# Kernel optimization log

Hardware: AMD Instinct MI355X
Metric: run time of the kernel (lower is better)

The kernel has to match this reference:

```python
import jax, jax.numpy as jnp
import numpy as np

B, S, H, V = 2, 2048, 1024, 32000
SDS = [64, 128, 256]
EPS = 1e-5


def _ln(x, g, b):
    m = jnp.mean(x, -1, keepdims=True)
    v = jnp.var(x, -1, keepdims=True)
    return (x - m) * jax.lax.rsqrt(v + EPS) * g + b


def _layer(x, A_log, Wb, Wc, D, Wg, bg, Wo, bo, g, be):
    # x: [B,S,H]; state dim N = A_log.shape[0]
    A = jnp.exp(A_log)
    gate = jax.nn.sigmoid(jnp.einsum('bsh,nh->bsn', x, Wg) + bg)
    Bx = jnp.einsum('bsh,nh->bsn', x, Wb)
    u = gate * Bx  # [B,S,N]

    def step(s, u_t):
        s = A * s + u_t
        return s, s

    s0 = jnp.zeros((x.shape[0], A.shape[0]), x.dtype)
    _, states = jax.lax.scan(step, s0, jnp.swapaxes(u, 0, 1))  # [S,B,N]
    states = jnp.swapaxes(states, 0, 1)
    y = jnp.einsum('bsn,hn->bsh', states, Wc) + D * x
    out = _ln(y + x, g, be)
    return out @ Wo.T + bo  # dropout is identity (p used in eval / p=0)


def setup_inputs() -> dict:
    key = jax.random.key(0)
    ks = iter(jax.random.split(key, 64))
    d = {}
    d['x'] = jax.random.randint(next(ks), (B, S), 0, V)
    d['E'] = jax.random.normal(next(ks), (V, H), jnp.float32) * 0.02
    for i, N in enumerate(SDS):
        d[f'A{i}'] = jnp.log(jnp.exp(jnp.full((N,), -0.5)) + 0.1 * jax.random.normal(next(ks), (N,)))
        d[f'Wb{i}'] = jax.random.normal(next(ks), (N, H), jnp.float32) * 0.02
        d[f'Wc{i}'] = jax.random.normal(next(ks), (H, N), jnp.float32) * 0.02
        d[f'D{i}'] = jax.random.normal(next(ks), (H,), jnp.float32)
        d[f'Wg{i}'] = jax.random.normal(next(ks), (N, H), jnp.float32) * 0.02
        d[f'bg{i}'] = jnp.zeros((N,), jnp.float32)
        d[f'Wo{i}'] = jax.random.normal(next(ks), (H, H), jnp.float32) * 0.02
        d[f'bo{i}'] = jnp.zeros((H,), jnp.float32)
        d[f'g{i}'] = jnp.ones((H,), jnp.float32)
        d[f'be{i}'] = jnp.zeros((H,), jnp.float32)
    d['Wf'] = jax.random.normal(next(ks), (H, 3 * H), jnp.float32) * 0.02
    d['bf'] = jnp.zeros((H,), jnp.float32)
    d['gf'] = jnp.ones((H,), jnp.float32)
    d['bef'] = jnp.zeros((H,), jnp.float32)
    d['Wh'] = jax.random.normal(next(ks), (V, H), jnp.float32) * 0.02
    d['bh'] = jnp.zeros((V,), jnp.float32)
    return d


def reference(x, E,
              A0, Wb0, Wc0, D0, Wg0, bg0, Wo0, bo0, g0, be0,
              A1, Wb1, Wc1, D1, Wg1, bg1, Wo1, bo1, g1, be1,
              A2, Wb2, Wc2, D2, Wg2, bg2, Wo2, bo2, g2, be2,
              Wf, bf, gf, bef, Wh, bh):
    emb = E[x]  # [B,S,H]
    o0 = _layer(emb, A0, Wb0, Wc0, D0, Wg0, bg0, Wo0, bo0, g0, be0)
    o1 = _layer(emb, A1, Wb1, Wc1, D1, Wg1, bg1, Wo1, bo1, g1, be1)
    o2 = _layer(emb, A2, Wb2, Wc2, D2, Wg2, bg2, Wo2, bo2, g2, be2)
    combined = jnp.concatenate([o0, o1, o2], axis=-1)  # [B,S,3H]
    fused = combined @ Wf.T + bf
    fused = _ln(fused + emb, gf, bef)
    logits = fused @ Wh.T + bh  # [B,S,V]
    return logits
```

## Files before the change

### kernel.cpp

```cpp
#include <hip/hip_runtime.h>
#include <hip/hip_bf16.h>

#define Hd 1024
#define Bdim 2
#define Sd 2048
#define BSd 4096
#define Vd 32000
#define EPSf 1e-5f
#define CH 16
#define NCH 128
#define NT3 448

typedef __attribute__((ext_vector_type(8))) short short8;
typedef __attribute__((ext_vector_type(4))) float f32x4;
typedef __attribute__((ext_vector_type(4))) unsigned short us4;

__device__ __forceinline__ unsigned short f2bf(float f) {
  union { float f; unsigned int u; } v; v.f = f;
  return (unsigned short)((v.u + 0x7fffu + ((v.u >> 16) & 1u)) >> 16);
}

typedef __attribute__((address_space(1))) const void gvoid_t;
typedef __attribute__((address_space(3))) void svoid_t;
__device__ __forceinline__ void gl_lds16(const void* g, void* s) {
  __builtin_amdgcn_global_load_lds((gvoid_t*)g, (svoid_t*)s, 16, 0, 0);
}

struct CvtTab {
  const float* src[14];
  unsigned short* dst[14];
  int start[15];
};
__global__ void k_cvt_all(CvtTab tab) {
  int b = blockIdx.x;
  int j = 0;
  while (j < 13 && b >= tab.start[j + 1]) ++j;
  size_t i = (size_t)(b - tab.start[j]) * 256 + threadIdx.x;
  f32x4 v = *(const f32x4*)(tab.src[j] + i * 4);
  us4 o;
  o[0] = f2bf(v[0]); o[1] = f2bf(v[1]); o[2] = f2bf(v[2]); o[3] = f2bf(v[3]);
  *(us4*)(tab.dst[j] + i * 4) = o;
}

__global__ void k_setup(const float* A0, const float* A1, const float* A2,
                        const float* b0, const float* b1, const float* b2,
                        const float* D0, const float* D1, const float* D2,
                        const float* g0, const float* g1, const float* g2,
                        const float* e0, const float* e1, const float* e2,
                        float* Alog448, float* bg448,
                        float* D3, float* g3, float* be3) {
  int t = blockIdx.x * 256 + threadIdx.x;
  if (t < NT3) {
    int l = t < 64 ? 0 : (t < 192 ? 1 : 2);
    int o = t - (l == 0 ? 0 : (l == 1 ? 64 : 192));
    Alog448[t] = (l == 0 ? A0 : (l == 1 ? A1 : A2))[o];
    bg448[t]   = (l == 0 ? b0 : (l == 1 ? b1 : b2))[o];
  }
  if (t < 3072) {
    int l = t >> 10, o = t & 1023;
    D3[t]  = (l == 0 ? D0 : (l == 1 ? D1 : D2))[o];
    g3[t]  = (l == 0 ? g0 : (l == 1 ? g1 : g2))[o];
    be3[t] = (l == 0 ? e0 : (l == 1 ? e1 : e2))[o];
  }
}

__global__ void k_embed(const int* __restrict__ x, const float* __restrict__ E,
                        float* __restrict__ emb, unsigned short* __restrict__ embbf) {
  int row = blockIdx.x, t = threadIdx.x;
  int id = x[row];
  f32x4 v = *(const f32x4*)(E + (size_t)id * Hd + t * 4);
  *(f32x4*)(emb + (size_t)row * Hd + t * 4) = v;
  us4 o;
  o[0] = f2bf(v[0]); o[1] = f2bf(v[1]); o[2] = f2bf(v[2]); o[3] = f2bf(v[3]);
  *(us4*)(embbf + (size_t)row * Hd + t * 4) = o;
}

template<int BM, int BN, int WM, int WN, int BF16_OUT>
__launch_bounds__(WM * WN * 64)
__global__ void gemm2ph(const unsigned short* __restrict__ A,
                        const unsigned short* __restrict__ Bw,
                        const float* __restrict__ bias,
                        void* __restrict__ Cv,
                        int N, int K, int lda, int ldb, int ldc, int coff, int tm)
{
  constexpr int NT = WM * WN * 64;
  constexpr int MF = BM / WM / 16;
  constexpr int NF = BN / WN / 16;
  constexpr int ASZ = BM * 64;
  constexpr int BSZ = BN * 64;
  constexpr int AR = (ASZ * 2) / (NT * 16);
  constexpr int BR = (BSZ * 2) / (NT * 16);
  __shared__ __align__(16) unsigned short Sm[2 * (ASZ + BSZ)];

  int T = gridDim.x;
  int orig = blockIdx.x;
  int q = T >> 3, r = T & 7;
  int xc = orig & 7, sdv = orig >> 3;
  int wgid = (xc < r ? xc * (q + 1) : r * (q + 1) + (xc - r) * q) + sdv;
  int n_t = wgid / tm, m_t = wgid % tm;
  int row0 = m_t * BM, col0 = n_t * BN;

  int tid = threadIdx.x;
  int wave = tid >> 6, lane = tid & 63;
  int wm = wave / WN, wn = wave % WN;
  int wr = wm * (BM / WM), wc = wn * (BN / WN);
  int lr = lane & 15;
  int klane = lane >> 4;

  f32x4 acc[MF][NF] = {};

  auto stage = [&](int buf, int k0) {
    unsigned short* Ab = Sm + buf * (ASZ + BSZ);
    unsigned short* Bb = Ab + ASZ;
    #pragma unroll
    for (int j = 0; j < AR; ++j) {
      int slot = j * NT + tid;
      int lrow = slot >> 3, c16 = slot & 7;
      int scol = (c16 ^ (lrow & 7)) * 8;
      gl_lds16(A + (size_t)(row0 + lrow) * lda + k0 + scol, Ab + (j * NT + wave * 64) * 8);
    }
    #pragma unroll
    for (int j = 0; j < BR; ++j) {
      int slot = j * NT + tid;
      int lrow = slot >> 3, c16 = slot & 7;
      int scol = (c16 ^ (lrow & 7)) * 8;
      int brow = col0 + lrow;
      if (brow >= N) brow = N - 1;
      gl_lds16(Bw + (size_t)brow * ldb + k0 + scol, Bb + (j * NT + wave * 64) * 8);
    }
  };

  auto compute = [&](int buf) {
    const unsigned short* Ab = Sm + buf * (ASZ + BSZ);
    const unsigned short* Bb = Ab + ASZ;
    #pragma unroll
    for (int kk = 0; kk < 2; ++kk) {
      short8 afr[MF], bfr[NF];
      #pragma unroll
      for (int m = 0; m < MF; ++m) {
        int row = wr + m * 16 + lr;
        int cs = (kk * 4 + klane) ^ (row & 7);
        afr[m] = *(const short8*)(Ab + row * 64 + cs * 8);
      }
      #pragma unroll
      for (int n = 0; n < NF; ++n) {
        int row = wc + n * 16 + lr;
        int cs = (kk * 4 + klane) ^ (row & 7);
        bfr[n] = *(const short8*)(Bb + row * 64 + cs * 8);
      }
      #pragma unroll
      for (int m = 0; m < MF; ++m)
        #pragma unroll
        for (int n = 0; n < NF; ++n)
          acc[m][n] = __builtin_amdgcn_mfma_f32_16x16x32_bf16(afr[m], bfr[n], acc[m][n], 0, 0, 0);
    }
  };

  int nt = K >> 6;
  stage(0, 0);
  __syncthreads();
  for (int t = 0; t < nt - 1; ++t) {
    stage((t & 1) ^ 1, (t + 1) * 64);
    compute(t & 1);
    __syncthreads();
  }
  compute((nt - 1) & 1);

  int rb = (lane >> 4) * 4;
  #pragma unroll
  for (int m = 0; m < MF; ++m) {
    #pragma unroll
    for (int n = 0; n < NF; ++n) {
      int gcol = col0 + wc + n * 16 + lr;
      if (gcol >= N) continue;
      float bv = bias ? bias[gcol] : 0.f;
      #pragma unroll
      for (int j = 0; j < 4; ++j) {
        int grow = row0 + wr + m * 16 + rb + j;
        float val = acc[m][n][j] + bv;
        if (BF16_OUT)
          ((unsigned short*)Cv)[(size_t)grow * ldc + coff + gcol] = f2bf(val);
        else
          ((float*)Cv)[(size_t)grow * ldc + coff + gcol] = val;
      }
    }
  }
}

__global__ void k_scanA(const float* __restrict__ gzbx, const float* __restrict__ Alog448,
                        const float* __restrict__ bg448,
                        float* __restrict__ st, float* __restrict__ carry) {
  int gid = blockIdx.x * 256 + threadIdx.x;
  if (gid >= Bdim * NCH * NT3) return;
  int n = gid % NT3;
  int c = (gid / NT3) % NCH;
  int b = gid / (NT3 * NCH);
  float a = expf(Alog448[n]);
  float bgv = bg448[n];
  float s = 0.f;
  size_t rbase = (size_t)b * Sd + (size_t)c * CH;
  for (int t = 0; t < CH; ++t) {
    size_t row = rbase + t;
    float gzv = gzbx[row * 896 + n];
    float bxv = gzbx[row * 896 + 448 + n];
    float gv = 1.f / (1.f + expf(-(gzv + bgv)));
    s = a * s + gv * bxv;
    st[row * NT3 + n] = s;
  }
  carry[((size_t)b * NCH + c) * NT3 + n] = s;
}

__global__ void k_scanB(const float* __restrict__ carry, const float* __restrict__ Alog448,
                        float* __restrict__ cin) {
  int i = blockIdx.x * 256 + threadIdx.x;
  if (i >= Bdim * NT3) return;
  int b = i / NT3, n = i % NT3;
  float aC = expf((float)CH * Alog448[n]);
  float s = 0.f;
  for (int c = 0; c < NCH; ++c) {
    cin[((size_t)b * NCH + c) * NT3 + n] = s;
    s = aC * s + carry[((size_t)b * NCH + c) * NT3 + n];
  }
}

__global__ void k_scanC(const float* __restrict__ st, const float* __restrict__ cin,
                        const float* __restrict__ Alog448, unsigned short* __restrict__ stbf) {
  size_t gid = (size_t)blockIdx.x * 256 + threadIdx.x;
  if (gid >= (size_t)BSd * NT3) return;
  int n = gid % NT3;
  int row = gid / NT3;
  int b = row / Sd, sg = row % Sd;
  int c = sg / CH, t = sg % CH;
  float cv = cin[((size_t)b * NCH + c) * NT3 + n];
  float val = st[gid] + expf((float)(t + 1) * Alog448[n]) * cv;
  stbf[gid] = f2bf(val);
}

__global__ void k_ln3(const float* __restrict__ y3, const float* __restrict__ emb,
                      const float* __restrict__ D3, const float* __restrict__ g3,
                      const float* __restrict__ be3, unsigned short* __restrict__ z3) {
  int row = blockIdx.x, ly = blockIdx.y, t = threadIdx.x;
  const float* y = y3 + (size_t)row * 3072 + ly * 1024;
  f32x4 yv = *(const f32x4*)(y + t * 4);
  f32x4 ev = *(const f32x4*)(emb + (size_t)row * Hd + t * 4);
  float vals[4];
  float sum = 0.f, sq = 0.f;
  #pragma unroll
  for (int j = 0; j < 4; ++j) {
    float coef = D3[ly * 1024 + t * 4 + j] + 1.f;
    float v = yv[j] + coef * ev[j];
    vals[j] = v; sum += v; sq += v * v;
  }
  #pragma unroll
  for (int o = 32; o >= 1; o >>= 1) {
    sum += __shfl_xor(sum, o);
    sq += __shfl_xor(sq, o);
  }
  __shared__ float red[2][4];
  int w = t >> 6, lane = t & 63;
  if (lane == 0) { red[0][w] = sum; red[1][w] = sq; }
  __syncthreads();
  sum = red[0][0] + red[0][1] + red[0][2] + red[0][3];
  sq  = red[1][0] + red[1][1] + red[1][2] + red[1][3];
  float mean = sum * (1.f / Hd);
  float var = sq * (1.f / Hd) - mean * mean;
  float rs = rsqrtf(var + EPSf);
  us4 o4;
  #pragma unroll
  for (int j = 0; j < 4; ++j) {
    float z = (vals[j] - mean) * rs * g3[ly * 1024 + t * 4 + j] + be3[ly * 1024 + t * 4 + j];
    o4[j] = f2bf(z);
  }
  *(us4*)(z3 + (size_t)row * 3072 + ly * 1024 + t * 4) = o4;
}

__global__ void k_ln(const float* __restrict__ y, const float* __restrict__ emb,
                     const float* __restrict__ g, const float* __restrict__ be,
                     unsigned short* __restrict__ out) {
  int row = blockIdx.x, t = threadIdx.x;
  f32x4 yv = *(const f32x4*)(y + (size_t)row * Hd + t * 4);
  f32x4 ev = *(const f32x4*)(emb + (size_t)row * Hd + t * 4);
  float vals[4];
  float sum = 0.f, sq = 0.f;
  #pragma unroll
  for (int j = 0; j < 4; ++j) {
    float v = yv[j] + ev[j];
    vals[j] = v; sum += v; sq += v * v;
  }
  #pragma unroll
  for (int o = 32; o >= 1; o >>= 1) {
    sum += __shfl_xor(sum, o);
    sq += __shfl_xor(sq, o);
  }
  __shared__ float red[2][4];
  int w = t >> 6, lane = t & 63;
  if (lane == 0) { red[0][w] = sum; red[1][w] = sq; }
  __syncthreads();
  sum = red[0][0] + red[0][1] + red[0][2] + red[0][3];
  sq  = red[1][0] + red[1][1] + red[1][2] + red[1][3];
  float mean = sum * (1.f / Hd);
  float var = sq * (1.f / Hd) - mean * mean;
  float rs = rsqrtf(var + EPSf);
  us4 o4;
  #pragma unroll
  for (int j = 0; j < 4; ++j) {
    float z = (vals[j] - mean) * rs * g[t * 4 + j] + be[t * 4 + j];
    o4[j] = f2bf(z);
  }
  *(us4*)(out + (size_t)row * Hd + t * 4) = o4;
}

extern "C" void kernel_launch(void* const* d_in, const int* in_sizes, int n_in,
                              void* d_out, int out_size, void* d_ws, size_t ws_size,
                              hipStream_t stream) {
  (void)in_sizes; (void)n_in; (void)out_size; (void)ws_size;
  const int* x = (const int*)d_in[0];
  const float* E = (const float*)d_in[1];
  const float* Wf_ = (const float*)d_in[32];
  const float* bfb = (const float*)d_in[33];
  const float* gfp = (const float*)d_in[34];
  const float* bef = (const float*)d_in[35];
  const float* Wh_ = (const float*)d_in[36];
  const float* bh = (const float*)d_in[37];

  char* wsb = (char*)d_ws;
  size_t off = 0;
  auto alloc = [&](size_t bytes) -> void* {
    void* p = wsb + off;
    off += (bytes + 255) & ~(size_t)255;
    return p;
  };
  float* emb             = (float*)alloc((size_t)BSd * Hd * 4);
  unsigned short* embbf  = (unsigned short*)alloc((size_t)BSd * Hd * 2);
  unsigned short* wgwbbf = (unsigned short*)alloc((size_t)896 * Hd * 2);
  unsigned short* wcbf   = (unsigned short*)alloc((size_t)NT3 * Hd * 2);
  unsigned short* wobf   = (unsigned short*)alloc((size_t)3 * Hd * Hd * 2);
  unsigned short* wfbf   = (unsigned short*)alloc((size_t)3 * Hd * Hd * 2);
  unsigned short* whbf   = (unsigned short*)alloc((size_t)Vd * Hd * 2);
  float* gzbx            = (float*)alloc((size_t)BSd * 896 * 4);
  float* stl             = (float*)alloc((size_t)BSd * NT3 * 4);
  unsigned short* stbf   = (unsigned short*)alloc((size_t)BSd * NT3 * 2);
  float* carry           = (float*)alloc((size_t)Bdim * NCH * NT3 * 4);
  float* cin             = (float*)alloc((size_t)Bdim * NCH * NT3 * 4);
  float* ybuf3           = (float*)alloc((size_t)BSd * 3072 * 4);
  unsigned short* zbf3   = (unsigned short*)alloc((size_t)BSd * 3072 * 2);
  unsigned short* zbf    = (unsigned short*)alloc((size_t)BSd * Hd * 2);
  unsigned short* combbf = (unsigned short*)alloc((size_t)BSd * 3072 * 2);
  float* Alog448         = (float*)alloc(NT3 * 4);
  float* bg448           = (float*)alloc(NT3 * 4);
  float* D3              = (float*)alloc(3072 * 4);
  float* g3              = (float*)alloc(3072 * 4);
  float* be3             = (float*)alloc(3072 * 4);

  k_embed<<<BSd, 256, 0, stream>>>(x, E, emb, embbf);

  {
    CvtTab tab;
    const int rowoff_g[3] = {0, 64, 192};
    int j = 0;
    int n4s[14];
    for (int i = 0; i < 3; ++i) { tab.src[j] = (const float*)d_in[2 + 10 * i + 4]; tab.dst[j] = wgwbbf + (size_t)rowoff_g[i] * Hd;        n4s[j] = (64 << i) * Hd / 4; ++j; }
    for (int i = 0; i < 3; ++i) { tab.src[j] = (const float*)d_in[2 + 10 * i + 1]; tab.dst[j] = wgwbbf + (size_t)(448 + rowoff_g[i]) * Hd; n4s[j] = (64 << i) * Hd / 4; ++j; }
    for (int i = 0; i < 3; ++i) { tab.src[j] = (const float*)d_in[2 + 10 * i + 2]; tab.dst[j] = wcbf + (size_t)rowoff_g[i] * Hd;           n4s[j] = (64 << i) * Hd / 4; ++j; }
    for (int i = 0; i < 3; ++i) { tab.src[j] = (const float*)d_in[2 + 10 * i + 6]; tab.dst[j] = wobf + (size_t)i * Hd * Hd;                n4s[j] = Hd * Hd / 4; ++j; }
    tab.src[j] = Wf_; tab.dst[j] = wfbf; n4s[j] = 3 * Hd * Hd / 4; ++j;
    tab.src[j] = Wh_; tab.dst[j] = whbf; n4s[j] = Vd * Hd / 4; ++j;
    tab.start[0] = 0;
    for (int k = 0; k < 14; ++k) tab.start[k + 1] = tab.start[k] + (n4s[k] + 255) / 256;
    k_cvt_all<<<tab.start[14], 256, 0, stream>>>(tab);
  }

  k_setup<<<12, 256, 0, stream>>>(
      (const float*)d_in[2], (const float*)d_in[12], (const float*)d_in[22],
      (const float*)d_in[7], (const float*)d_in[17], (const float*)d_in[27],
      (const float*)d_in[5], (const float*)d_in[15], (const float*)d_in[25],
      (const float*)d_in[10], (const float*)d_in[20], (const float*)d_in[30],
      (const float*)d_in[11], (const float*)d_in[21], (const float*)d_in[31],
      Alog448, bg448, D3, g3, be3);

  const int TM = BSd / 128;

  gemm2ph<128,128,2,2,0><<<(896 / 128) * TM, 256, 0, stream>>>(
      embbf, wgwbbf, nullptr, gzbx, 896, Hd, Hd, Hd, 896, 0, TM);

  {
    int totA = Bdim * NCH * NT3;
    k_scanA<<<(totA + 255) / 256, 256, 0, stream>>>(gzbx, Alog448, bg448, stl, carry);
    k_scanB<<<(Bdim * NT3 + 255) / 256, 256, 0, stream>>>(carry, Alog448, cin);
    size_t totC = (size_t)BSd * NT3;
    k_scanC<<<(int)((totC + 255) / 256), 256, 0, stream>>>(stl, cin, Alog448, stbf);
  }

  const int owg[3] = {0, 64, 192};
  const int sd[3] = {64, 128, 256};
  for (int i = 0; i < 3; ++i) {
    gemm2ph<128,128,2,2,0><<<(Hd / 128) * TM, 256, 0, stream>>>(
        stbf + owg[i], wcbf + (size_t)owg[i] * Hd, nullptr, ybuf3,
        Hd, sd[i], NT3, sd[i], 3072, i * Hd, TM);
  }

  k_ln3<<<dim3(BSd, 3), 256, 0, stream>>>(ybuf3, emb, D3, g3, be3, zbf3);

  for (int i = 0; i < 3; ++i) {
    const float* bo = (const float*)d_in[2 + 10 * i + 7];
    gemm2ph<128,128,2,2,1><<<(Hd / 128) * TM, 256, 0, stream>>>(
        zbf3 + i * Hd, wobf + (size_t)i * Hd * Hd, bo, combbf,
        Hd, Hd, 3072, Hd, 3072, i * Hd, TM);
  }

  gemm2ph<128,128,2,2,0><<<(Hd / 128) * TM, 256, 0, stream>>>(
      combbf, wfbf, bfb, ybuf3, Hd, 3 * Hd, 3 * Hd, 3 * Hd, Hd, 0, TM);
  k_ln<<<BSd, 256, 0, stream>>>(ybuf3, emb, gfp, bef, zbf);

  const int TM256 = BSd / 256;
  gemm2ph<256,256,2,4,0><<<(Vd / 256) * TM256, 512, 0, stream>>>(
      zbf, whbf, bh, (float*)d_out, Vd, Hd, Hd, Hd, Vd, 0, TM256);
}
```

Measured before the change: 671.6 us.

## Fold per-layer output projections into fusion weights; add 4-stage pipelined vocab GEMM

Precomputes a combined weight Wf·blockdiag(Wo_i) and a combined bias (bf + Wf·bo), so the three per-layer 1024x1024 output GEMMs over 4096 tokens go away. Their cost is replaced by small weight-only GEMMs plus a transpose-convert kernel. The final vocab projection also moves to a new 256x256 GEMM with a 4-buffer LDS ring that issues async global-to-LDS loads three stages ahead, using XCD-aware block remapping and setprio around the MFMAs. The risk is extra bf16 rounding in the combined weight, plus more LDS use per block in the ring GEMM.

```diff
diff --git a/kernel.cpp b/kernel.cpp
--- a/kernel.cpp
+++ b/kernel.cpp
@@ -27,19 +27,52 @@
 }
 
 struct CvtTab {
-  const float* src[14];
-  unsigned short* dst[14];
-  int start[15];
+  const float* src[11];
+  unsigned short* dst[11];
+  int start[12];
 };
 __global__ void k_cvt_all(CvtTab tab) {
   int b = blockIdx.x;
   int j = 0;
-  while (j < 13 && b >= tab.start[j + 1]) ++j;
+  while (j < 10 && b >= tab.start[j + 1]) ++j;
   size_t i = (size_t)(b - tab.start[j]) * 256 + threadIdx.x;
   f32x4 v = *(const f32x4*)(tab.src[j] + i * 4);
   us4 o;
   o[0] = f2bf(v[0]); o[1] = f2bf(v[1]); o[2] = f2bf(v[2]); o[3] = f2bf(v[3]);
   *(us4*)(tab.dst[j] + i * 4) = o;
+}
+
+__global__ void k_cvtT(const float* __restrict__ s0, const float* __restrict__ s1,
+                       const float* __restrict__ s2, unsigned short* __restrict__ dst) {
+  const float* src = blockIdx.z == 0 ? s0 : (blockIdx.z == 1 ? s1 : s2);
+  unsigned short* d = dst + (size_t)blockIdx.z * Hd * Hd;
+  __shared__ float tile[32][33];
+  int tx = threadIdx.x & 31, ty = threadIdx.x >> 5;
+  int bx = blockIdx.x * 32, by = blockIdx.y * 32;
+  #pragma unroll
+  for (int i = 0; i < 4; ++i)
+    tile[ty + i * 8][tx] = src[(size_t)(by + ty + i * 8) * Hd + bx + tx];
+  __syncthreads();
+  #pragma unroll
+  for (int i = 0; i < 4; ++i)
+    d[(size_t)(bx + ty + i * 8) * Hd + by + tx] = f2bf(tile[tx][ty + i * 8]);
+}
+
+__global__ void k_biasf(const float* __restrict__ Wf_, const float* __restrict__ bfb,
+                        const float* __restrict__ bo0, const float* __restrict__ bo1,
+                        const float* __restrict__ bo2, float* __restrict__ biasf) {
+  int h = blockIdx.x, t = threadIdx.x;
+  float s = 0.f;
+  for (int c = t; c < 3072; c += 256) {
+    float b = c < 1024 ? bo0[c] : (c < 2048 ? bo1[c - 1024] : bo2[c - 2048]);
+    s += Wf_[(size_t)h * 3072 + c] * b;
+  }
+  #pragma unroll
+  for (int o = 32; o >= 1; o >>= 1) s += __shfl_xor(s, o);
+  __shared__ float red[4];
+  if ((t & 63) == 0) red[t >> 6] = s;
+  __syncthreads();
+  if (t == 0) biasf[h] = bfb[h] + red[0] + red[1] + red[2] + red[3];
 }
 
 __global__ void k_setup(const float* A0, const float* A1, const float* A2,
@@ -187,6 +220,100 @@
   }
 }
 
+__launch_bounds__(512)
+__global__ void gemm_ring(const unsigned short* __restrict__ A,
+                          const unsigned short* __restrict__ Bw,
+                          const float* __restrict__ bias,
+                          float* __restrict__ Cv,
+                          int N, int K, int lda, int ldb, int ldc, int tm)
+{
+  constexpr int ASZ = 256 * 32;
+  constexpr int BUF = 2 * ASZ;
+  __shared__ __align__(16) unsigned short Sm[4 * BUF];
+
+  int T = gridDim.x;
+  int orig = blockIdx.x;
+  int q = T >> 3, r = T & 7;
+  int xc = orig & 7, sdv = orig >> 3;
+  int wgid = (xc < r ? xc * (q + 1) : r * (q + 1) + (xc - r) * q) + sdv;
+  int n_t = wgid / tm, m_t = wgid % tm;
+  int row0 = m_t * 256, col0 = n_t * 256;
+
+  int tid = threadIdx.x;
+  int wave = tid >> 6, lane = tid & 63;
+  int wm = wave >> 2, wn = wave & 3;
+  int wr = wm * 128, wc = wn * 64;
+  int lr = lane & 15, klane = lane >> 4;
+
+  f32x4 acc[8][4] = {};
+
+  auto stage = [&](int buf, int kt) {
+    int k0 = kt * 32;
+    unsigned short* Ab = Sm + buf * BUF;
+    unsigned short* Bb = Ab + ASZ;
+    #pragma unroll
+    for (int j = 0; j < 2; ++j) {
+      int slot = j * 512 + wave * 64 + lane;
+      int rrow = slot >> 2, ck = (slot & 3) * 8;
+      gl_lds16(A + (size_t)(row0 + rrow) * lda + k0 + ck, Ab + (j * 512 + wave * 64) * 8);
+    }
+    #pragma unroll
+    for (int j = 0; j < 2; ++j) {
+      int slot = j * 512 + wave * 64 + lane;
+      int rrow = slot >> 2, ck = (slot & 3) * 8;
+      int brow = col0 + rrow;
+      if (brow >= N) brow = N - 1;
+      gl_lds16(Bw + (size_t)brow * ldb + k0 + ck, Bb + (j * 512 + wave * 64) * 8);
+    }
+  };
+
+  auto compute = [&](int buf) {
+    const unsigned short* Ab = Sm + buf * BUF;
+    const unsigned short* Bb = Ab + ASZ;
+    short8 afr[8], bfr[4];
+    #pragma unroll
+    for (int m = 0; m < 8; ++m)
+      afr[m] = *(const short8*)(Ab + (wr + m * 16 + lr) * 32 + klane * 8);
+    #pragma unroll
+    for (int n = 0; n < 4; ++n)
+      bfr[n] = *(const short8*)(Bb + (wc + n * 16 + lr) * 32 + klane * 8);
+    __builtin_amdgcn_s_setprio(1);
+    #pragma unroll
+    for (int m = 0; m < 8; ++m)
+      #pragma unroll
+      for (int n = 0; n < 4; ++n)
+        acc[m][n] = __builtin_amdgcn_mfma_f32_16x16x32_bf16(afr[m], bfr[n], acc[m][n], 0, 0, 0);
+    __builtin_amdgcn_s_setprio(0);
+  };
+
+  int nt = K >> 5;
+  stage(0, 0); stage(1, 1); stage(2, 2);
+  for (int t = 0; t < nt; ++t) {
+    if (t < nt - 2)       asm volatile("s_waitcnt vmcnt(8)" ::: "memory");
+    else if (t == nt - 2) asm volatile("s_waitcnt vmcnt(4)" ::: "memory");
+    else                  asm volatile("s_waitcnt vmcnt(0)" ::: "memory");
+    __builtin_amdgcn_s_barrier();
+    if (t + 3 < nt) stage((t + 3) & 3, t + 3);
+    compute(t & 3);
+  }
+
+  int rb = (lane >> 4) * 4;
+  #pragma unroll
+  for (int m = 0; m < 8; ++m) {
+    #pragma unroll
+    for (int n = 0; n < 4; ++n) {
+      int gcol = col0 + wc + n * 16 + lr;
+      if (gcol >= N) continue;
+      float bv = bias ? bias[gcol] : 0.f;
+      #pragma unroll
+      for (int j = 0; j < 4; ++j) {
+        int grow = row0 + wr + m * 16 + rb + j;
+        Cv[(size_t)grow * ldc + gcol] = acc[m][n][j] + bv;
+      }
+    }
+  }
+}
+
 __global__ void k_scanA(const float* __restrict__ gzbx, const float* __restrict__ Alog448,
                         const float* __restrict__ bg448,
                         float* __restrict__ st, float* __restrict__ carry) {
@@ -334,8 +461,9 @@
   unsigned short* embbf  = (unsigned short*)alloc((size_t)BSd * Hd * 2);
   unsigned short* wgwbbf = (unsigned short*)alloc((size_t)896 * Hd * 2);
   unsigned short* wcbf   = (unsigned short*)alloc((size_t)NT3 * Hd * 2);
-  unsigned short* wobf   = (unsigned short*)alloc((size_t)3 * Hd * Hd * 2);
+  unsigned short* wotbf  = (unsigned short*)alloc((size_t)3 * Hd * Hd * 2);
   unsigned short* wfbf   = (unsigned short*)alloc((size_t)3 * Hd * Hd * 2);
+  unsigned short* wcombbf= (unsigned short*)alloc((size_t)Hd * 3 * Hd * 2);
   unsigned short* whbf   = (unsigned short*)alloc((size_t)Vd * Hd * 2);
   float* gzbx            = (float*)alloc((size_t)BSd * 896 * 4);
   float* stl             = (float*)alloc((size_t)BSd * NT3 * 4);
@@ -345,12 +473,12 @@
   float* ybuf3           = (float*)alloc((size_t)BSd * 3072 * 4);
   unsigned short* zbf3   = (unsigned short*)alloc((size_t)BSd * 3072 * 2);
   unsigned short* zbf    = (unsigned short*)alloc((size_t)BSd * Hd * 2);
-  unsigned short* combbf = (unsigned short*)alloc((size_t)BSd * 3072 * 2);
   float* Alog448         = (float*)alloc(NT3 * 4);
   float* bg448           = (float*)alloc(NT3 * 4);
   float* D3              = (float*)alloc(3072 * 4);
   float* g3              = (float*)alloc(3072 * 4);
   float* be3             = (float*)alloc(3072 * 4);
+  float* biasf           = (float*)alloc(Hd * 4);
 
   k_embed<<<BSd, 256, 0, stream>>>(x, E, emb, embbf);
 
@@ -358,17 +486,19 @@
     CvtTab tab;
     const int rowoff_g[3] = {0, 64, 192};
     int j = 0;
-    int n4s[14];
-    for (int i = 0; i < 3; ++i) { tab.src[j] = (const float*)d_in[2 + 10 * i + 4]; tab.dst[j] = wgwbbf + (size_t)rowoff_g[i] * Hd;        n4s[j] = (64 << i) * Hd / 4; ++j; }
-    for (int i = 0; i < 3; ++i) { tab.src[j] = (const float*)d_in[2 + 10 * i + 1]; tab.dst[j] = wgwbbf + (size_t)(448 + rowoff_g[i]) * Hd; n4s[j] = (64 << i) * Hd / 4; ++j; }
-    for (int i = 0; i < 3; ++i) { tab.src[j] = (const float*)d_in[2 + 10 * i + 2]; tab.dst[j] = wcbf + (size_t)rowoff_g[i] * Hd;           n4s[j] = (64 << i) * Hd / 4; ++j; }
-    for (int i = 0; i < 3; ++i) { tab.src[j] = (const float*)d_in[2 + 10 * i + 6]; tab.dst[j] = wobf + (size_t)i * Hd * Hd;                n4s[j] = Hd * Hd / 4; ++j; }
+    int n4s[11];
+    for (int i = 0; i < 3; ++i) { tab.src[j] = (const float*)d_in[2 + 10 * i + 4]; tab.dst[j] = wgwbbf + (size_t)rowoff_g[i] * Hd;         n4s[j] = (64 << i) * Hd / 4; ++j; }
+    for (int i = 0; i < 3; ++i) { tab.src[j] = (const float*)d_in[2 + 10 * i + 1]; tab.dst[j] = wgwbbf + (size_t)(448 + rowoff_g[i]) * Hd;  n4s[j] = (64 << i) * Hd / 4; ++j; }
+    for (int i = 0; i < 3; ++i) { tab.src[j] = (const float*)d_in[2 + 10 * i + 2]; tab.dst[j] = wcbf + (size_t)rowoff_g[i] * Hd;            n4s[j] = (64 << i) * Hd / 4; ++j; }
     tab.src[j] = Wf_; tab.dst[j] = wfbf; n4s[j] = 3 * Hd * Hd / 4; ++j;
     tab.src[j] = Wh_; tab.dst[j] = whbf; n4s[j] = Vd * Hd / 4; ++j;
     tab.start[0] = 0;
-    for (int k = 0; k < 14; ++k) tab.start[k + 1] = tab.start[k] + (n4s[k] + 255) / 256;
-    k_cvt_all<<<tab.start[14], 256, 0, stream>>>(tab);
-  }
+    for (int k = 0; k < 11; ++k) tab.start[k + 1] = tab.start[k] + (n4s[k] + 255) / 256;
+    k_cvt_all<<<tab.start[11], 256, 0, stream>>>(tab);
+  }
+
+  k_cvtT<<<dim3(32, 32, 3), 256, 0, stream>>>(
+      (const float*)d_in[8], (const float*)d_in[18], (const float*)d_in[28], wotbf);
 
   k_setup<<<12, 256, 0, stream>>>(
       (const float*)d_in[2], (const float*)d_in[12], (const float*)d_in[22],
@@ -378,6 +508,15 @@
       (const float*)d_in[11], (const float*)d_in[21], (const float*)d_in[31],
       Alog448, bg448, D3, g3, be3);
 
+  k_biasf<<<Hd, 256, 0, stream>>>(Wf_, bfb,
+      (const float*)d_in[9], (const float*)d_in[19], (const float*)d_in[29], biasf);
+
+  for (int i = 0; i < 3; ++i) {
+    gemm2ph<128,128,2,2,1><<<(Hd / 128) * (Hd / 128), 256, 0, stream>>>(
+        wfbf + i * Hd, wotbf + (size_t)i * Hd * Hd, nullptr, wcombbf,
+        Hd, Hd, 3 * Hd, Hd, 3 * Hd, i * Hd, Hd / 128);
+  }
+
   const int TM = BSd / 128;
 
   gemm2ph<128,128,2,2,0><<<(896 / 128) * TM, 256, 0, stream>>>(
@@ -401,18 +540,11 @@
 
   k_ln3<<<dim3(BSd, 3), 256, 0, stream>>>(ybuf3, emb, D3, g3, be3, zbf3);
 
-  for (int i = 0; i < 3; ++i) {
-    const float* bo = (const float*)d_in[2 + 10 * i + 7];
-    gemm2ph<128,128,2,2,1><<<(Hd / 128) * TM, 256, 0, stream>>>(
-        zbf3 + i * Hd, wobf + (size_t)i * Hd * Hd, bo, combbf,
-        Hd, Hd, 3072, Hd, 3072, i * Hd, TM);
-  }
-
   gemm2ph<128,128,2,2,0><<<(Hd / 128) * TM, 256, 0, stream>>>(
-      combbf, wfbf, bfb, ybuf3, Hd, 3 * Hd, 3 * Hd, 3 * Hd, Hd, 0, TM);
+      zbf3, wcombbf, biasf, ybuf3, Hd, 3 * Hd, 3 * Hd, 3 * Hd, Hd, 0, TM);
   k_ln<<<BSd, 256, 0, stream>>>(ybuf3, emb, gfp, bef, zbf);
 
   const int TM256 = BSd / 256;
-  gemm2ph<256,256,2,4,0><<<(Vd / 256) * TM256, 512, 0, stream>>>(
-      zbf, whbf, bh, (float*)d_out, Vd, Hd, Hd, Hd, Vd, 0, TM256);
-}
+  gemm_ring<<<(Vd / 256) * TM256, 512, 0, stream>>>(
+      zbf, whbf, bh, (float*)d_out, Vd, Hd, Hd, Hd, Vd, TM256);
+}
```

Measured after the change: 648.7 us. -3.4%, faster.
